# Performance work log

Hardware: AMD Instinct MI355X
Metric: run time of the kernel (lower is better)

The kernel has to match this reference:

```python
import math
import jax, jax.numpy as jnp
import numpy as np

HIDDEN = 128
NUM_REL = 48
NUM_BASES = 8
NUM_ENT = 50000
NUM_SPECIAL = 64
NUM_EDGES = 600000


def setup_inputs() -> dict:
    key = jax.random.key(0)
    ks = jax.random.split(key, 8)
    edge_index = jax.random.randint(ks[0], (2, NUM_EDGES), 0, NUM_ENT, dtype=jnp.int64)
    edge_type = jax.random.randint(ks[1], (NUM_EDGES,), 0, NUM_REL, dtype=jnp.int64)
    # node embeddings: uniform(-stdv, stdv), stdv = sqrt(6/(N+d)) as in the torch init
    stdv = math.sqrt(6.0 / (NUM_ENT + HIDDEN))
    node_embeds = jax.random.uniform(ks[2], (NUM_ENT, HIDDEN), jnp.float32, -stdv, stdv)
    # RGCN basis-decomposition params (PyG RGCNConv): weight [B, d, d], comp [R, B]
    basis = jax.random.normal(ks[3], (NUM_BASES, HIDDEN, HIDDEN), jnp.float32) * (1.0 / math.sqrt(HIDDEN))
    comp = jax.random.normal(ks[4], (NUM_REL, NUM_BASES), jnp.float32) * (1.0 / math.sqrt(NUM_BASES))
    root = jax.random.normal(ks[5], (HIDDEN, HIDDEN), jnp.float32) * (1.0 / math.sqrt(HIDDEN))
    bias = jnp.zeros((HIDDEN,), jnp.float32)
    special_emb = jax.random.normal(ks[6], (NUM_SPECIAL, HIDDEN), jnp.float32) * 0.02
    special_emb = special_emb.at[0].set(0.0)  # padding_idx=0
    return {"edge_index": edge_index, "edge_type": edge_type,
            "node_embeds": node_embeds, "basis": basis, "comp": comp,
            "root": root, "bias": bias, "special_emb": special_emb}


def rgcn_conv(x, edge_index, edge_type, basis, comp, root, bias):
    # PyG RGCNConv with basis decomposition, aggr='mean', root weight + bias.
    # W_r = sum_b comp[r, b] * basis[b]; out[n] = x[n] @ root + bias
    #        + sum_r mean_{e: type(e)=r, dst(e)=n} (x[src(e)] @ W_r)
    N = x.shape[0]
    R, B = comp.shape
    src, dst = edge_index[0], edge_index[1]
    # per-(relation, dst) in-degree for the per-relation mean aggregation
    seg = edge_type * N + dst  # [E]
    cnt = jax.ops.segment_sum(jnp.ones(src.shape[0], x.dtype), seg, num_segments=R * N)
    norm = 1.0 / jnp.maximum(cnt[seg], 1.0)  # [E]
    w = comp[edge_type] * norm[:, None]  # [E, B] per-edge basis coefficients / count
    x_src = x[src]  # [E, d] gather (dominant memory traffic)
    out = x @ root + bias  # [N, d]
    # linearity: mean over edges of (x_src @ W) == (weighted-sum of x_src) @ basis_b per basis
    for b in range(B):
        agg = jax.ops.segment_sum(x_src * w[:, b:b + 1], dst, num_segments=N)  # [N, d]
        out = out + agg @ basis[b]
    return out


def reference(edge_index, edge_type, node_embeds, basis, comp, root, bias, special_emb):
    node_out = rgcn_conv(node_embeds, edge_index, edge_type, basis, comp, root, bias)
    return jnp.concatenate([node_out, special_emb], axis=0)  # [N + S, d]
```

## Files before the change

### kernel.cpp

```cpp
#include <hip/hip_runtime.h>

#define NDIM 128
#define NBASES 8
#define KDIM 1152
#define GTILE 16
#define APITCH 1160

typedef __attribute__((ext_vector_type(8))) __bf16 bfrag;
typedef __attribute__((ext_vector_type(4))) float f32x4;

__device__ __forceinline__ float bf2f(unsigned short b) {
    return __uint_as_float(((unsigned)b) << 16);
}
__device__ __forceinline__ unsigned short f2bf(float f) {
    unsigned u = __float_as_uint(f);
    unsigned r = u + 0x7FFFu + ((u >> 16) & 1u);
    return (unsigned short)(r >> 16);
}
__device__ __forceinline__ unsigned pack2bf(float lo, float hi) {
    return (unsigned)f2bf(lo) | ((unsigned)f2bf(hi) << 16);
}
__device__ __forceinline__ float loadF(const void* p, int idx, int isf32) {
    return isf32 ? ((const float*)p)[idx] : bf2f(((const unsigned short*)p)[idx]);
}

__global__ void detect_k(const unsigned short* __restrict__ xs,
                         const int* __restrict__ ei, int* __restrict__ meta) {
    if (threadIdx.x != 0 || blockIdx.x != 0) return;
    const uint4* xv = (const uint4*)xs;
    unsigned f32m = 0;
    uint4 bx[16];
    #pragma unroll
    for (int i = 0; i < 16; ++i) bx[i] = xv[i];
    #pragma unroll
    for (int i = 0; i < 16; ++i) {
        unsigned a = bx[i].x, b = bx[i].y, c = bx[i].z, d = bx[i].w;
        f32m |= (((a & 0xFFFFu) >> 7) & 0xFFu) > 124u;
        f32m |= (((b & 0xFFFFu) >> 7) & 0xFFu) > 124u;
        f32m |= (((c & 0xFFFFu) >> 7) & 0xFFu) > 124u;
        f32m |= (((d & 0xFFFFu) >> 7) & 0xFFu) > 124u;
    }
    const uint4* ev = (const uint4*)ei;
    unsigned nzm = 0;
    for (int r = 0; r < 4; ++r) {
        uint4 be[16];
        #pragma unroll
        for (int i = 0; i < 16; ++i) be[i] = ev[r * 16 + i];
        #pragma unroll
        for (int i = 0; i < 16; ++i) nzm |= be[i].y | be[i].w;
    }
    meta[0] = f32m ? 1 : 0;
    meta[1] = nzm ? 0 : 1;
}

__global__ void misc_k(const void* __restrict__ basis, const void* __restrict__ root,
                       const void* __restrict__ se, const int* __restrict__ meta,
                       unsigned short* __restrict__ BT, void* __restrict__ out,
                       int scount, int sbase,
                       const int* __restrict__ ei, int E, int N, int* __restrict__ hist) {
    int t = blockIdx.x * 256 + threadIdx.x;
    int isf32 = meta[0];
    if (t < NDIM * KDIM) {
        int j = t / KDIM, k = t % KDIM;
        float v = (k < NBASES * NDIM) ? loadF(basis, k * NDIM + j, isf32)
                                      : loadF(root, (k - NBASES * NDIM) * NDIM + j, isf32);
        BT[t] = f2bf(v);
    } else {
        int u = t - NDIM * KDIM;
        if (u < scount) {
            float v = loadF(se, u, isf32);
            if (isf32) ((float*)out)[sbase + u] = v;
            else       ((unsigned short*)out)[sbase + u] = f2bf(v);
        } else {
            int e = u - scount;
            if (e < E) {
                int dst = meta[1] ? ei[2 * (E + e)] : ei[E + e];
                dst = min(max(dst, 0), N - 1);
                atomicAdd(&hist[dst], 1);
            }
        }
    }
}

__global__ void scanA_k(const int* __restrict__ hist, int N,
                        int* __restrict__ offsets, int* __restrict__ bsum) {
    __shared__ int s[1024];
    int tid = threadIdx.x;
    int idx = blockIdx.x * 1024 + tid;
    int v = (idx < N) ? hist[idx] : 0;
    s[tid] = v;
    __syncthreads();
    for (int off = 1; off < 1024; off <<= 1) {
        int t = 0;
        if (tid >= off) t = s[tid - off];
        __syncthreads();
        if (tid >= off) s[tid] += t;
        __syncthreads();
    }
    if (idx < N) offsets[idx] = s[tid] - v;
    if (tid == 1023) bsum[blockIdx.x] = s[1023];
}
__global__ void scanB_k(const int* __restrict__ bsum, int NB, int N,
                        int* __restrict__ bpre, int* __restrict__ offsets) {
    __shared__ int s[64];
    int tid = threadIdx.x;
    int v = (tid < NB) ? bsum[tid] : 0;
    s[tid] = v;
    __syncthreads();
    for (int off = 1; off < 64; off <<= 1) {
        int t = 0;
        if (tid >= off) t = s[tid - off];
        __syncthreads();
        if (tid >= off) s[tid] += t;
        __syncthreads();
    }
    if (tid < NB) bpre[tid] = s[tid] - v;
    if (tid == NB - 1) offsets[N] = s[tid];
}

__global__ void scatter_k(const int* __restrict__ ei, const int* __restrict__ et,
                          int E, int N, const int* __restrict__ meta,
                          const int* __restrict__ offsets, const int* __restrict__ bpre,
                          int* __restrict__ cursor, int* __restrict__ sorted) {
    int e = blockIdx.x * 256 + threadIdx.x;
    if (e >= E) return;
    int i64 = meta[1];
    int src = i64 ? ei[2 * e] : ei[e];
    int dst = i64 ? ei[2 * (E + e)] : ei[E + e];
    int rel = i64 ? et[2 * e] : et[e];
    src = min(max(src, 0), N - 1);
    dst = min(max(dst, 0), N - 1);
    rel = rel & 63;
    int pos = offsets[dst] + bpre[dst >> 10] + atomicAdd(&cursor[dst], 1);
    sorted[pos] = src | (rel << 16);
}

__global__ __launch_bounds__(1024, 8) void rgcn_main_k(
    const void* __restrict__ x, const void* __restrict__ comp,
    const void* __restrict__ bias, const unsigned short* __restrict__ BT,
    const int* __restrict__ meta, const int* __restrict__ offsets,
    const int* __restrict__ bpre,
    const int* __restrict__ sorted, void* __restrict__ out, int N)
{
    __shared__ alignas(16) unsigned short A_lds[GTILE * APITCH];
    __shared__ alignas(16) float comp_lds[48 * NBASES];
    __shared__ int cnt_lds[GTILE * 48];
    const int tid  = threadIdx.x;
    const int lane = tid & 63;
    const int wave = tid >> 6;
    const int isf32 = meta[0];

    for (int t = tid; t < 48 * NBASES; t += 1024)
        comp_lds[t] = loadF(comp, t, isf32);
    __syncthreads();

    const int nodeBase = blockIdx.x * GTILE;
    const int dl = lane & 31;
    const int eg = lane >> 5;

    {
        const int n = nodeBase + wave;
        float acc[4][4];
        #pragma unroll
        for (int b = 0; b < 4; ++b)
            #pragma unroll
            for (int i = 0; i < 4; ++i) acc[b][i] = 0.f;

        int* cnt_row = &cnt_lds[wave * 48];

        if (n < N) {
            const int start = offsets[n] + bpre[n >> 10];
            const int idx1  = n + 1;
            const int end   = offsets[idx1] + ((idx1 < N) ? bpre[idx1 >> 10] : 0);

            if (lane < 48) cnt_row[lane] = 0;
            for (int c = start + lane; c < end; c += 64)
                atomicAdd(&cnt_row[(sorted[c] >> 16) & 63], 1);
            if (lane < 48) {
                float nv = __builtin_amdgcn_rcpf(fmaxf((float)cnt_row[lane], 1.0f));
                cnt_row[lane] = __float_as_int(nv);
            }

            if (!isf32) {
                const unsigned short* xh = (const unsigned short*)x;
                if (start < end) {
                    unsigned q0 = (start + eg     < end) ? (unsigned)sorted[start + eg]     : 0u;
                    unsigned q1 = (start + 2 + eg < end) ? (unsigned)sorted[start + 2 + eg] : 0u;
                    unsigned q2 = (start + 4 + eg < end) ? (unsigned)sorted[start + 4 + eg] : 0u;
                    unsigned q3 = (start + 6 + eg < end) ? (unsigned)sorted[start + 6 + eg] : 0u;
                    uint2 xa0 = *(const uint2*)(xh + (size_t)(q0 & 0xFFFFu) * NDIM + dl * 4);
                    uint2 xa1 = *(const uint2*)(xh + (size_t)(q1 & 0xFFFFu) * NDIM + dl * 4);
                    uint2 xa2 = *(const uint2*)(xh + (size_t)(q2 & 0xFFFFu) * NDIM + dl * 4);
                    uint2 xa3 = *(const uint2*)(xh + (size_t)(q3 & 0xFFFFu) * NDIM + dl * 4);
                    unsigned q4 = (start + 8 + eg < end) ? (unsigned)sorted[start + 8 + eg] : 0u;
                    for (int c = start; c < end; c += 2) {
                        uint2 xa4 = *(const uint2*)(xh + (size_t)(q4 & 0xFFFFu) * NDIM + dl * 4);
                        unsigned q5 = (c + 10 + eg < end) ? (unsigned)sorted[c + 10 + eg] : 0u;

                        bool act_o = (c + eg) < end;
                        bool act_p = (c + (1 ^ eg)) < end;
                        unsigned qp = (unsigned)__shfl_xor((int)q0, 32);
                        int rel_o = (int)((q0 >> 16) & 63u);
                        int rel_p = (int)((qp >> 16) & 63u);
                        float nrm_o = act_o ? __int_as_float(cnt_row[rel_o]) : 0.f;
                        float nrm_p = act_p ? __int_as_float(cnt_row[rel_p]) : 0.f;
                        f32x4 cw_o = *(const f32x4*)&comp_lds[rel_o * NBASES + 4 * eg];
                        f32x4 cw_p = *(const f32x4*)&comp_lds[rel_p * NBASES + 4 * eg];
                        unsigned px = (unsigned)__shfl_xor((int)xa0.x, 32);
                        unsigned py = (unsigned)__shfl_xor((int)xa0.y, 32);
                        float xo[4], xq[4];
                        xo[0] = __uint_as_float(xa0.x << 16)          * nrm_o;
                        xo[1] = __uint_as_float(xa0.x & 0xFFFF0000u)  * nrm_o;
                        xo[2] = __uint_as_float(xa0.y << 16)          * nrm_o;
                        xo[3] = __uint_as_float(xa0.y & 0xFFFF0000u)  * nrm_o;
                        xq[0] = __uint_as_float(px << 16)             * nrm_p;
                        xq[1] = __uint_as_float(px & 0xFFFF0000u)     * nrm_p;
                        xq[2] = __uint_as_float(py << 16)             * nrm_p;
                        xq[3] = __uint_as_float(py & 0xFFFF0000u)     * nrm_p;
                        #pragma unroll
                        for (int b = 0; b < 4; ++b)
                            #pragma unroll
                            for (int i = 0; i < 4; ++i)
                                acc[b][i] += cw_o[b] * xo[i] + cw_p[b] * xq[i];
                        q0 = q1; q1 = q2; q2 = q3; q3 = q4; q4 = q5;
                        xa0 = xa1; xa1 = xa2; xa2 = xa3; xa3 = xa4;
                    }
                }
            } else {
                const float* xfp = (const float*)x;
                for (int c = start; c < end; c += 2) {
                    bool act_o = (c + eg) < end;
                    bool act_p = (c + (1 ^ eg)) < end;
                    int io = c + eg;
                    unsigned q0 = (io < end) ? (unsigned)sorted[io] : 0u;
                    unsigned qp = (unsigned)__shfl_xor((int)q0, 32);
                    int rel_o = (int)((q0 >> 16) & 63u);
                    int rel_p = (int)((qp >> 16) & 63u);
                    float nrm_o = act_o ? __int_as_float(cnt_row[rel_o]) : 0.f;
                    float nrm_p = act_p ? __int_as_float(cnt_row[rel_p]) : 0.f;
                    f32x4 cw_o = *(const f32x4*)&comp_lds[rel_o * NBASES + 4 * eg];
                    f32x4 cw_p = *(const f32x4*)&comp_lds[rel_p * NBASES + 4 * eg];
                    f32x4 xv = *(const f32x4*)(xfp + (size_t)(q0 & 0xFFFFu) * NDIM + dl * 4);
                    float xo[4], xq[4];
                    #pragma unroll
                    for (int i = 0; i < 4; ++i) {
                        xo[i] = xv[i] * nrm_o;
                        xq[i] = __shfl_xor(xv[i], 32) * nrm_p;
                    }
                    #pragma unroll
                    for (int b = 0; b < 4; ++b)
                        #pragma unroll
                        for (int i = 0; i < 4; ++i)
                            acc[b][i] += cw_o[b] * xo[i] + cw_p[b] * xq[i];
                }
            }
        }

        unsigned short* row = &A_lds[wave * APITCH];
        #pragma unroll
        for (int b = 0; b < 4; ++b) {
            uint2 p;
            p.x = pack2bf(acc[b][0], acc[b][1]);
            p.y = pack2bf(acc[b][2], acc[b][3]);
            *(uint2*)(row + (4 * eg + b) * NDIM + dl * 4) = p;
        }
        if (eg == 0) {
            uint2 xr = {0, 0};
            if (n < N) {
                if (!isf32) {
                    xr = *(const uint2*)((const unsigned short*)x + (size_t)n * NDIM + dl * 4);
                } else {
                    const float* xf = (const float*)x + (size_t)n * NDIM + dl * 4;
                    xr.x = pack2bf(xf[0], xf[1]);
                    xr.y = pack2bf(xf[2], xf[3]);
                }
            }
            *(uint2*)(row + NBASES * NDIM + dl * 4) = xr;
        }
    }
    __syncthreads();

    if (wave < 4) {
        const int m = lane & 15;
        const int q = lane >> 4;
        f32x4 C0 = {0,0,0,0}, C1 = {0,0,0,0};
        const unsigned short* arow = &A_lds[m * APITCH];
        const int jb = wave * 32;
        for (int ks = 0; ks < KDIM / 32; ++ks) {
            int k = ks * 32 + q * 8;
            bfrag a  = *(const bfrag*)(arow + k);
            bfrag b0 = *(const bfrag*)(BT + (size_t)(jb +  0 + m) * KDIM + k);
            bfrag b1 = *(const bfrag*)(BT + (size_t)(jb + 16 + m) * KDIM + k);
            C0 = __builtin_amdgcn_mfma_f32_16x16x32_bf16(a, b0, C0, 0, 0, 0);
            C1 = __builtin_amdgcn_mfma_f32_16x16x32_bf16(a, b1, C1, 0, 0, 0);
        }
        #pragma unroll
        for (int t = 0; t < 2; ++t) {
            f32x4 Ct = t ? C1 : C0;
            int j = jb + t * 16 + m;
            float bj = loadF(bias, j, isf32);
            #pragma unroll
            for (int r = 0; r < 4; ++r) {
                int n = nodeBase + q * 4 + r;
                if (n < N) {
                    float v = Ct[r] + bj;
                    if (isf32) ((float*)out)[(size_t)n * NDIM + j] = v;
                    else       ((unsigned short*)out)[(size_t)n * NDIM + j] = f2bf(v);
                }
            }
        }
    }
}

extern "C" void kernel_launch(void* const* d_in, const int* in_sizes, int n_in,
                              void* d_out, int out_size, void* d_ws, size_t ws_size,
                              hipStream_t stream) {
    const int* ei = (const int*)d_in[0];
    const int* et = (const int*)d_in[1];

    const int E = in_sizes[1];
    const int N = in_sizes[2] / NDIM;
    const int S = in_sizes[7] / NDIM;
    const int NB = (N + 1023) / 1024;

    char* ws = (char*)d_ws;
    size_t off = 0;
    int* meta    = (int*)(ws + off); off += 16;
    int* hist    = (int*)(ws + off); off += (size_t)N * 4;
    int* cursor  = (int*)(ws + off); off += (size_t)N * 4;
    int* offsets = (int*)(ws + off); off = (off + (size_t)(N + 1) * 4 + 15) & ~(size_t)15;
    int* bsum    = (int*)(ws + off); off += 64 * 4;
    int* bpre    = (int*)(ws + off); off += 64 * 4;
    unsigned short* BT = (unsigned short*)(ws + off); off += (size_t)NDIM * KDIM * 2;
    int* sorted  = (int*)(ws + off); off += (size_t)E * 4;

    hipMemsetAsync(hist, 0, (size_t)2 * N * 4, stream);

    detect_k<<<1, 64, 0, stream>>>((const unsigned short*)d_in[2], ei, meta);
    {
        int T = NDIM * KDIM + S * NDIM + E;
        misc_k<<<(T + 255) / 256, 256, 0, stream>>>(
            d_in[3], d_in[5], d_in[7], meta, BT, d_out, S * NDIM, N * NDIM,
            ei, E, N, hist);
    }
    scanA_k<<<NB, 1024, 0, stream>>>(hist, N, offsets, bsum);
    scanB_k<<<1, 64, 0, stream>>>(bsum, NB, N, bpre, offsets);
    scatter_k<<<(E + 255) / 256, 256, 0, stream>>>(ei, et, E, N, meta, offsets, bpre, cursor, sorted);
    rgcn_main_k<<<(N + GTILE - 1) / GTILE, 1024, 0, stream>>>(d_in[2], d_in[4], d_in[6], BT,
                                                              meta, offsets, bpre, sorted, d_out, N);
}
```

Baseline: 322.4 us.

## Fuse preprocessing kernels into one cooperative kernel with grid syncs

Merges the misc/histogram, two-level scan, and scatter kernels into a single cooperative launch of 256 blocks of 1024 threads, using grid.sync() between phases. This removes three kernel launches and their inter-kernel gaps. In exchange, work runs on a fixed grid with grid-stride loops, grid-wide barriers add their own cost, and the scatter and histogram phases get less parallelism than before.

```diff
diff --git a/kernel.cpp b/kernel.cpp
--- a/kernel.cpp
+++ b/kernel.cpp
@@ -1,10 +1,14 @@
 #include <hip/hip_runtime.h>
+#include <hip/hip_cooperative_groups.h>
+
+namespace cg = cooperative_groups;
 
 #define NDIM 128
 #define NBASES 8
 #define KDIM 1152
 #define GTILE 16
 #define APITCH 1160
+#define PREGRID 256
 
 typedef __attribute__((ext_vector_type(8))) __bf16 bfrag;
 typedef __attribute__((ext_vector_type(4))) float f32x4;
@@ -53,86 +57,92 @@
     meta[1] = nzm ? 0 : 1;
 }
 
-__global__ void misc_k(const void* __restrict__ basis, const void* __restrict__ root,
-                       const void* __restrict__ se, const int* __restrict__ meta,
-                       unsigned short* __restrict__ BT, void* __restrict__ out,
-                       int scount, int sbase,
-                       const int* __restrict__ ei, int E, int N, int* __restrict__ hist) {
-    int t = blockIdx.x * 256 + threadIdx.x;
-    int isf32 = meta[0];
-    if (t < NDIM * KDIM) {
-        int j = t / KDIM, k = t % KDIM;
-        float v = (k < NBASES * NDIM) ? loadF(basis, k * NDIM + j, isf32)
-                                      : loadF(root, (k - NBASES * NDIM) * NDIM + j, isf32);
-        BT[t] = f2bf(v);
-    } else {
-        int u = t - NDIM * KDIM;
-        if (u < scount) {
+__global__ __launch_bounds__(1024, 1) void pre_k(
+    const void* __restrict__ basis, const void* __restrict__ root,
+    const void* __restrict__ se, const int* __restrict__ meta,
+    unsigned short* __restrict__ BT, void* __restrict__ out,
+    int scount, int sbase,
+    const int* __restrict__ ei, const int* __restrict__ et,
+    int E, int N, int NB,
+    int* __restrict__ hist, int* __restrict__ offsets,
+    int* __restrict__ bsum, int* __restrict__ bpre,
+    int* __restrict__ cursor, int* __restrict__ sorted)
+{
+    cg::grid_group grid = cg::this_grid();
+    __shared__ int s[1024];
+    const int tid  = threadIdx.x;
+    const int gtid = blockIdx.x * 1024 + tid;
+    const int gsz  = gridDim.x * 1024;
+    const int isf32 = meta[0];
+    const int i64   = meta[1];
+
+    for (int t = gtid; t < NDIM * KDIM + scount; t += gsz) {
+        if (t < NDIM * KDIM) {
+            int j = t / KDIM, k = t % KDIM;
+            float v = (k < NBASES * NDIM) ? loadF(basis, k * NDIM + j, isf32)
+                                          : loadF(root, (k - NBASES * NDIM) * NDIM + j, isf32);
+            BT[t] = f2bf(v);
+        } else {
+            int u = t - NDIM * KDIM;
             float v = loadF(se, u, isf32);
             if (isf32) ((float*)out)[sbase + u] = v;
             else       ((unsigned short*)out)[sbase + u] = f2bf(v);
-        } else {
-            int e = u - scount;
-            if (e < E) {
-                int dst = meta[1] ? ei[2 * (E + e)] : ei[E + e];
-                dst = min(max(dst, 0), N - 1);
-                atomicAdd(&hist[dst], 1);
-            }
-        }
-    }
-}
-
-__global__ void scanA_k(const int* __restrict__ hist, int N,
-                        int* __restrict__ offsets, int* __restrict__ bsum) {
-    __shared__ int s[1024];
-    int tid = threadIdx.x;
-    int idx = blockIdx.x * 1024 + tid;
-    int v = (idx < N) ? hist[idx] : 0;
-    s[tid] = v;
-    __syncthreads();
-    for (int off = 1; off < 1024; off <<= 1) {
-        int t = 0;
-        if (tid >= off) t = s[tid - off];
+        }
+    }
+    for (int e = gtid; e < E; e += gsz) {
+        int dst = i64 ? ei[2 * (E + e)] : ei[E + e];
+        dst = min(max(dst, 0), N - 1);
+        atomicAdd(&hist[dst], 1);
+    }
+    grid.sync();
+
+    for (int w = blockIdx.x; w < NB; w += gridDim.x) {
         __syncthreads();
-        if (tid >= off) s[tid] += t;
+        int idx = w * 1024 + tid;
+        int v = (idx < N) ? hist[idx] : 0;
+        s[tid] = v;
         __syncthreads();
-    }
-    if (idx < N) offsets[idx] = s[tid] - v;
-    if (tid == 1023) bsum[blockIdx.x] = s[1023];
-}
-__global__ void scanB_k(const int* __restrict__ bsum, int NB, int N,
-                        int* __restrict__ bpre, int* __restrict__ offsets) {
-    __shared__ int s[64];
-    int tid = threadIdx.x;
-    int v = (tid < NB) ? bsum[tid] : 0;
-    s[tid] = v;
-    __syncthreads();
-    for (int off = 1; off < 64; off <<= 1) {
-        int t = 0;
-        if (tid >= off) t = s[tid - off];
+        for (int off = 1; off < 1024; off <<= 1) {
+            int t = 0;
+            if (tid >= off) t = s[tid - off];
+            __syncthreads();
+            if (tid >= off) s[tid] += t;
+            __syncthreads();
+        }
+        if (idx < N) offsets[idx] = s[tid] - v;
+        if (tid == 1023) bsum[w] = s[1023];
+    }
+    grid.sync();
+
+    if (blockIdx.x == 0) {
+        int v = 0;
+        if (tid < 64) {
+            v = (tid < NB) ? bsum[tid] : 0;
+            s[tid] = v;
+        }
         __syncthreads();
-        if (tid >= off) s[tid] += t;
-        __syncthreads();
-    }
-    if (tid < NB) bpre[tid] = s[tid] - v;
-    if (tid == NB - 1) offsets[N] = s[tid];
-}
-
-__global__ void scatter_k(const int* __restrict__ ei, const int* __restrict__ et,
-                          int E, int N, const int* __restrict__ meta,
-                          const int* __restrict__ offsets, const int* __restrict__ bpre,
-                          int* __restrict__ cursor, int* __restrict__ sorted) {
-    int e = blockIdx.x * 256 + threadIdx.x;
-    if (e >= E) return;
-    int i64 = meta[1];
-    int src = i64 ? ei[2 * e] : ei[e];
-    int dst = i64 ? ei[2 * (E + e)] : ei[E + e];
-    int rel = i64 ? et[2 * e] : et[e];
-    src = min(max(src, 0), N - 1);
-    dst = min(max(dst, 0), N - 1);
-    rel = rel & 63;
-    int pos = offsets[dst] + bpre[dst >> 10] + atomicAdd(&cursor[dst], 1);
-    sorted[pos] = src | (rel << 16);
+        for (int off = 1; off < 64; off <<= 1) {
+            int t = 0;
+            if (tid >= off && tid < 64) t = s[tid - off];
+            __syncthreads();
+            if (tid >= off && tid < 64) s[tid] += t;
+            __syncthreads();
+        }
+        if (tid < NB) bpre[tid] = s[tid] - v;
+        if (tid == NB - 1) offsets[N] = s[tid];
+    }
+    grid.sync();
+
+    for (int e = gtid; e < E; e += gsz) {
+        int src = i64 ? ei[2 * e] : ei[e];
+        int dst = i64 ? ei[2 * (E + e)] : ei[E + e];
+        int rel = i64 ? et[2 * e] : et[e];
+        src = min(max(src, 0), N - 1);
+        dst = min(max(dst, 0), N - 1);
+        rel = rel & 63;
+        int pos = offsets[dst] + bpre[dst >> 10] + atomicAdd(&cursor[dst], 1);
+        sorted[pos] = src | (rel << 16);
+    }
 }
 
 __global__ __launch_bounds__(1024, 8) void rgcn_main_k(
@@ -301,11 +311,11 @@
             float bj = loadF(bias, j, isf32);
             #pragma unroll
             for (int r = 0; r < 4; ++r) {
-                int n = nodeBase + q * 4 + r;
-                if (n < N) {
+                int nn = nodeBase + q * 4 + r;
+                if (nn < N) {
                     float v = Ct[r] + bj;
-                    if (isf32) ((float*)out)[(size_t)n * NDIM + j] = v;
-                    else       ((unsigned short*)out)[(size_t)n * NDIM + j] = f2bf(v);
+                    if (isf32) ((float*)out)[(size_t)nn * NDIM + j] = v;
+                    else       ((unsigned short*)out)[(size_t)nn * NDIM + j] = f2bf(v);
                 }
             }
         }
@@ -337,15 +347,25 @@
     hipMemsetAsync(hist, 0, (size_t)2 * N * 4, stream);
 
     detect_k<<<1, 64, 0, stream>>>((const unsigned short*)d_in[2], ei, meta);
+
     {
-        int T = NDIM * KDIM + S * NDIM + E;
-        misc_k<<<(T + 255) / 256, 256, 0, stream>>>(
-            d_in[3], d_in[5], d_in[7], meta, BT, d_out, S * NDIM, N * NDIM,
-            ei, E, N, hist);
-    }
-    scanA_k<<<NB, 1024, 0, stream>>>(hist, N, offsets, bsum);
-    scanB_k<<<1, 64, 0, stream>>>(bsum, NB, N, bpre, offsets);
-    scatter_k<<<(E + 255) / 256, 256, 0, stream>>>(ei, et, E, N, meta, offsets, bpre, cursor, sorted);
+        const void* basis_p = d_in[3];
+        const void* root_p  = d_in[5];
+        const void* se_p    = d_in[7];
+        int scount = S * NDIM;
+        int sbase  = N * NDIM;
+        int E_ = E, N_ = N, NB_ = NB;
+        void* args[] = {
+            (void*)&basis_p, (void*)&root_p, (void*)&se_p, (void*)&meta,
+            (void*)&BT, (void*)&d_out, (void*)&scount, (void*)&sbase,
+            (void*)&ei, (void*)&et, (void*)&E_, (void*)&N_, (void*)&NB_,
+            (void*)&hist, (void*)&offsets, (void*)&bsum, (void*)&bpre,
+            (void*)&cursor, (void*)&sorted
+        };
+        hipLaunchCooperativeKernel((const void*)pre_k, dim3(PREGRID), dim3(1024),
+                                   args, 0, stream);
+    }
+
     rgcn_main_k<<<(N + GTILE - 1) / GTILE, 1024, 0, stream>>>(d_in[2], d_in[4], d_in[6], BT,
                                                               meta, offsets, bpre, sorted, d_out, N);
 }
```

After: 423.2 us. +31.3%, slower.
